# Kernel optimization log

Hardware: AMD Instinct MI355X
Metric: run time of the kernel (lower is better)

The kernel has to match this reference:

```python
import jax, jax.numpy as jnp
import numpy as np

B = 4096          # fused tokens (batch)
E = 1024          # attnConfig embed_size == MoE emb_size
OUT = E // 4      # per-branch feature dim (self.output)
N_EXP = 8         # number of experts
TOP = 2           # top-k routing
H = 8             # attention heads
HD = E // H       # head dim
HID = 4 * E       # expert MLP hidden
IMG = 64 * 64     # flattened single-channel image
W_IMP = 0.01      # importance loss weight


def setup_inputs() -> dict:
    key = jax.random.key(0)
    ks = jax.random.split(key, 24)
    n = lambda i, shp, sc=1.0: jax.random.normal(ks[i], shp, jnp.float32) * sc
    inp = {
        'source': n(0, (B, 1, 64, 64)),
        'target': n(1, (B, 1, 64, 64)),
        'background': n(2, (B, 1, 64, 64)),
        'image': n(3, (B, E)),
        'text': n(4, (B, E)),
        # shared encoder (stub: flatten -> fc to OUT, shared across s/t/b)
        'W_enc': n(5, (IMG, OUT), 0.02), 'b_enc': jnp.zeros((OUT,), jnp.float32),
        # linerImg
        'W_img': n(6, (E, OUT), 0.02), 'b_img': jnp.zeros((OUT,), jnp.float32),
        # cross attention
        'Wq': n(7, (E, E), 0.02), 'bq': jnp.zeros((E,), jnp.float32),
        'Wk': n(8, (E, E), 0.02), 'bk': jnp.zeros((E,), jnp.float32),
        'Wv': n(9, (E, E), 0.02), 'bv': jnp.zeros((E,), jnp.float32),
        'Wo': n(10, (E, E), 0.02), 'bo': jnp.zeros((E,), jnp.float32),
        # gate
        'W_gate': n(11, (E, N_EXP), 0.02), 'b_gate': jnp.zeros((N_EXP,), jnp.float32),
        # experts: per-expert 2-layer MLP E->HID->E
        'W1': n(12, (N_EXP, E, HID), 0.02), 'b1': jnp.zeros((N_EXP, HID), jnp.float32),
        'W2': n(13, (N_EXP, HID, E), 0.02), 'b2': jnp.zeros((N_EXP, E), jnp.float32),
    }
    return inp


def reference(source, target, background, image, text,
              W_enc, b_enc, W_img, b_img,
              Wq, bq, Wk, bk, Wv, bv, Wo, bo,
              W_gate, b_gate, W1, b1, W2, b2):
    enc = lambda a: a.reshape(a.shape[0], -1) @ W_enc + b_enc      # shared_encoder stub
    s = enc(source); t = enc(target); bg = enc(background)        # [B, OUT] each
    img = jax.nn.silu(image @ W_img + b_img)                      # [B, OUT]
    x = jnp.concatenate([s, t, bg, img], axis=1)                  # [B, E] visionFeatures

    # cross attention with seq_len 1 for both x (query) and text (key/value)
    q = (x @ Wq + bq).reshape(B, H, HD)
    k = (text @ Wk + bk).reshape(B, H, HD)
    v = (text @ Wv + bv).reshape(B, H, HD)
    scores = jnp.sum(q * k, axis=-1, keepdims=True) / jnp.sqrt(jnp.float32(HD))  # [B,H,1]
    attw = jax.nn.softmax(scores[..., None], axis=-1)[..., 0]     # softmax over 1 key == 1
    att = (attw * v).reshape(B, E) @ Wo + bo                       # [B, E]

    gate_logits = att @ W_gate + b_gate                            # [B, N_EXP]
    gate_prob = jax.nn.softmax(gate_logits, axis=-1)               # eval mode: no noise
    top_w, top_idx = jax.lax.top_k(gate_prob, TOP)                 # [B, TOP]
    top_w = jax.nn.softmax(top_w, axis=-1)                         # renormalize over top-k

    # dense-dispatch equivalent of the per-expert gather/index_add loop
    h = jax.nn.gelu(jnp.einsum('be,neh->nbh', x, W1) + b1[:, None, :])   # [N,B,HID]
    y_all = jnp.einsum('nbh,nhe->nbe', h, W2) + b2[:, None, :]           # [N,B,E]
    combine = jnp.zeros((B, N_EXP), jnp.float32).at[
        jnp.arange(B)[:, None], top_idx].add(top_w)                      # [B,N]
    y = jnp.einsum('nbe,bn->be', y_all, combine)                          # [B,E]

    importance = gate_prob.sum(axis=0)                             # [N_EXP]
    importance_loss = W_IMP * (jnp.std(importance, ddof=1) / jnp.mean(importance)) ** 2
    return (y, gate_prob, importance_loss)
```

## Files before the change

kernel.cpp:

```cpp
#include <hip/hip_runtime.h>
#include <hip/hip_bf16.h>
#include <stdint.h>

typedef __bf16 bf16_t;
typedef bf16_t bf16x8 __attribute__((ext_vector_type(8)));
typedef float f32x4 __attribute__((ext_vector_type(4)));

static constexpr int B_TOK  = 4096;
static constexpr int E_DIM  = 1024;
static constexpr int N_EXPC = 8;
static constexpr int HID    = 4096;
static constexpr int IMGSZ  = 4096;
static constexpr int NSLOT  = 2 * B_TOK;
static constexpr int NTIL   = 71;

#define DEVI __device__ __forceinline__

DEVI int imin(int a, int b) { return a < b ? a : b; }

DEVI uint16_t f2bf(float f) {
  union { float f; uint32_t u; } v; v.f = f;
  uint32_t u = v.u;
  return (uint16_t)((u + 0x7FFFu + ((u >> 16) & 1u)) >> 16);
}

DEVI void gload_lds16(const void* g, void* l) {
  __builtin_amdgcn_global_load_lds((const __attribute__((address_space(1))) void*)g,
                                   (__attribute__((address_space(3))) void*)l, 16, 0, 0);
}

template<int N> DEVI void waitv() {
  if constexpr (N == 0)       asm volatile("s_waitcnt vmcnt(0)" ::: "memory");
  else if constexpr (N == 2)  asm volatile("s_waitcnt vmcnt(2)" ::: "memory");
  else if constexpr (N == 4)  asm volatile("s_waitcnt vmcnt(4)" ::: "memory");
  else if constexpr (N == 5)  asm volatile("s_waitcnt vmcnt(5)" ::: "memory");
  else if constexpr (N == 8)  asm volatile("s_waitcnt vmcnt(8)" ::: "memory");
  else if constexpr (N == 10) asm volatile("s_waitcnt vmcnt(10)" ::: "memory");
}

#define BAR() do { __builtin_amdgcn_sched_barrier(0); __builtin_amdgcn_s_barrier(); \
                   __builtin_amdgcn_sched_barrier(0); } while (0)

#define MFMA16(a, b, c) __builtin_amdgcn_mfma_f32_16x16x32_bf16((a), (b), (c), 0, 0, 0)

__global__ __launch_bounds__(256)
void transpose64(const float* __restrict__ in, uint16_t* __restrict__ out, int R, int C)
{
  __shared__ float tile[64][65];
  size_t off = (size_t)blockIdx.z * (size_t)R * (size_t)C;
  int c0 = blockIdx.x * 64, r0 = blockIdx.y * 64;
  int t = threadIdx.x;
  #pragma unroll
  for (int i = 0; i < 16; ++i) {
    int rr = i * 4 + (t >> 6), cc = t & 63;
    tile[rr][cc] = in[off + (size_t)(r0 + rr) * C + c0 + cc];
  }
  __syncthreads();
  #pragma unroll
  for (int i = 0; i < 8; ++i) {
    int c = i * 8 + (t >> 5), j = t & 31;
    ushort2 w;
    w.x = f2bf(tile[2 * j][c]);
    w.y = f2bf(tile[2 * j + 1][c]);
    *(ushort2*)&out[off + (size_t)(c0 + c) * R + r0 + 2 * j] = w;
  }
}

template<int BN, int EPI, bool GATHER, bool TILED, int NT>
__global__ __launch_bounds__(256, 3)
void gemm_p(const uint16_t* __restrict__ Ab, int lda,
            const uint16_t* __restrict__ BT, void* __restrict__ Cv, int ldc,
            const float* __restrict__ bias, int K,
            const int* __restrict__ meta, const int* __restrict__ perm,
            size_t bStride, int biasStride)
{
  constexpr int HN = BN / 2, FN = BN / 32;
  constexpr int OPS = (BN == 128 ? 4 : 3);
  int rowBase, rows, e, nt;
  if constexpr (TILED) {
    constexpr int TOTAL = NTIL * NT, Q = TOTAL / 8, FULLB = 64 * NT;
    int bid = blockIdx.x;
    int wg = (bid & 7) * Q + (bid >> 3);
    int mtile;
    if (wg < FULLB) { int rem = wg % (8 * NT); mtile = (wg / (8 * NT)) * 8 + (rem & 7); nt = rem >> 3; }
    else            { int rem = wg - FULLB;    mtile = 64 + rem % 7;                    nt = rem / 7; }
    if (mtile >= meta[0]) return;
    e = meta[1 + 3 * mtile]; rowBase = meta[2 + 3 * mtile]; rows = meta[3 + 3 * mtile];
  } else {
    e = 0; rowBase = blockIdx.x * 128; rows = 128; nt = blockIdx.y;
  }
  const uint16_t* Bt = BT + (TILED ? (size_t)e * bStride : 0);
  const float* bi = bias + (TILED ? (size_t)e * (size_t)biasStride : 0);

  constexpr int ABUF = 8192;
  constexpr int BBUF = (BN == 128) ? 8192 : 4096;
  __shared__ __align__(16) char sAraw[3 * ABUF];
  __shared__ __align__(16) char sBraw[3 * BBUF];

  int t = threadIdx.x, wave = t >> 6, lane = t & 63;
  int wr = wave >> 1, wc = wave & 1;

  int rB = t >> 2;
  int slB = ((t & 3) ^ (rB & 3)) * 8;
  const uint16_t* gB0 = Bt + (size_t)(nt * BN + rB) * K + slB;
  const uint16_t* gB1 = Bt + (size_t)(nt * BN + rB + 64) * K + slB;

  int r0 = t >> 2, r1 = r0 + 64;
  int sl = ((t & 3) ^ (r0 & 3)) * 8;
  int car0, car1;
  if constexpr (TILED) {
    int rr0 = imin(r0, rows - 1), rr1 = imin(r1, rows - 1);
    car0 = GATHER ? perm[rowBase + rr0] : rowBase + rr0;
    car1 = GATHER ? perm[rowBase + rr1] : rowBase + rr1;
  } else { car0 = rowBase + r0; car1 = rowBase + r1; }
  const uint16_t* gA0 = Ab + (size_t)car0 * lda + sl;
  const uint16_t* gA1 = Ab + (size_t)car1 * lda + sl;

  char* laW = sAraw + wave * 1024;
  char* lbW = sBraw + wave * 1024;
  auto STAGE = [&](int kt, int c) {
    int ko = kt << 5;
    char* la = laW + c * ABUF;
    char* lb = lbW + c * BBUF;
    gload_lds16(gA0 + ko, la);
    gload_lds16(gA1 + ko, la + 4096);
    gload_lds16(gB0 + ko, lb);
    if constexpr (BN == 128) gload_lds16(gB1 + ko, lb + 4096);
  };

  f32x4 acc[4][FN];
  #pragma unroll
  for (int m = 0; m < 4; m++)
    #pragma unroll
    for (int n = 0; n < FN; n++)
      acc[m][n] = f32x4{0.f, 0.f, 0.f, 0.f};

  STAGE(0, 0);
  STAGE(1, 1);

  int fr = lane & 15;
  int rdoff = ((lane >> 4) ^ (lane & 3)) * 16;
  int c0 = 0, c2 = 2;
  int nk = K >> 5;

  for (int kt = 0; kt < nk; ++kt) {
    if (kt + 2 < nk) { STAGE(kt + 2, c2); waitv<2 * OPS>(); }
    else if (kt + 1 < nk) waitv<OPS>();
    else waitv<0>();
    BAR();

    const char* bA = sAraw + c0 * ABUF;
    const char* bB = sBraw + c0 * BBUF;
    bf16x8 af[4], bfr[FN];
    #pragma unroll
    for (int m = 0; m < 4; m++)
      af[m] = *(const bf16x8*)(bA + (wr * 64 + m * 16 + fr) * 64 + rdoff);
    #pragma unroll
    for (int n = 0; n < FN; n++)
      bfr[n] = *(const bf16x8*)(bB + (wc * HN + n * 16 + fr) * 64 + rdoff);
    #pragma unroll
    for (int m = 0; m < 4; m++)
      #pragma unroll
      for (int n = 0; n < FN; n++)
        acc[m][n] = MFMA16(af[m], bfr[n], acc[m][n]);

    BAR();
    c0 = (c0 == 2) ? 0 : c0 + 1;
    c2 = (c2 == 2) ? 0 : c2 + 1;
  }

  #pragma unroll
  for (int m = 0; m < 4; m++) {
    int lrow = wr * 64 + m * 16 + (lane >> 4) * 4;
    #pragma unroll
    for (int n = 0; n < FN; n++) {
      int col = nt * BN + wc * HN + n * 16 + (lane & 15);
      float bval = bi[col];
      #pragma unroll
      for (int r = 0; r < 4; r++) {
        int lr = lrow + r;
        if (TILED && lr >= rows) continue;
        float v = acc[m][n][r] + bval;
        size_t cr = (size_t)(rowBase + lr) * ldc + col;
        if (EPI == 3) {
          float u = v + 0.044715f * v * v * v;
          v = v / (1.f + __expf(-1.5957691216057308f * u));
          ((uint16_t*)Cv)[cr] = f2bf(v);
        } else {
          ((float*)Cv)[cr] = v;
        }
      }
    }
  }
}

template<int SPLITK>
__global__ __launch_bounds__(256, 3)
void gemm_encR(const float* __restrict__ F0, const float* __restrict__ F1,
               const float* __restrict__ F2, int lda,
               const uint16_t* __restrict__ BT, float* __restrict__ P, int K)
{
  int z = blockIdx.z, br = z / SPLITK, kc = z % SPLITK;
  const float* Af = (br == 0) ? F0 : (br == 1) ? F1 : F2;
  int Kc = K / SPLITK, k0 = kc * Kc;
  int rowBase = blockIdx.x * 64, nt = blockIdx.y;

  __shared__ __align__(16) char sB[3 * 8192];
  int t = threadIdx.x, wave = t >> 6, lane = t & 63;
  int fr = lane & 15, q4 = lane >> 4;

  const float* gA = Af + (size_t)(rowBase + wave * 16 + fr) * lda + k0 + q4 * 8;

  int rloc = t >> 2;
  int ssw = ((t & 3) ^ (rloc & 3)) * 8;
  const uint16_t* gB0 = BT + (size_t)(nt * 128 + rloc) * K + k0 + ssw;
  const uint16_t* gB1 = gB0 + (size_t)64 * K;

  auto STB = [&](int kt, int c) {
    gload_lds16(gB0 + kt * 32, sB + c * 8192 + wave * 1024);
    gload_lds16(gB1 + kt * 32, sB + c * 8192 + 4096 + wave * 1024);
  };

  f32x4 acc[8];
  #pragma unroll
  for (int n = 0; n < 8; ++n) acc[n] = f32x4{0.f, 0.f, 0.f, 0.f};

  int nk = Kc >> 5;
  STB(0, 0); STB(1, 1);
  f32x4 aE0 = *(const f32x4*)(gA),      aE1 = *(const f32x4*)(gA + 4);
  f32x4 aO0 = *(const f32x4*)(gA + 32), aO1 = *(const f32x4*)(gA + 36);
  int c0 = 0, c2 = 2;
  int bRow = (q4 ^ (fr & 3)) * 16;

  auto step = [&](int kt, f32x4& aX0, f32x4& aX1) {
    bool m2 = kt + 2 < nk;
    if (m2) STB(kt + 2, c2);
    bf16x8 a;
    a[0] = (bf16_t)aX0[0]; a[1] = (bf16_t)aX0[1]; a[2] = (bf16_t)aX0[2]; a[3] = (bf16_t)aX0[3];
    a[4] = (bf16_t)aX1[0]; a[5] = (bf16_t)aX1[1]; a[6] = (bf16_t)aX1[2]; a[7] = (bf16_t)aX1[3];
    int kp = m2 ? kt + 2 : kt;
    aX0 = *(const f32x4*)(gA + kp * 32);
    aX1 = *(const f32x4*)(gA + kp * 32 + 4);
    if (m2) waitv<10>(); else waitv<0>();
    BAR();
    const char* bb = sB + c0 * 8192;
    bf16x8 bfr[8];
    #pragma unroll
    for (int n = 0; n < 8; ++n)
      bfr[n] = *(const bf16x8*)(bb + n * 1024 + fr * 64 + bRow);
    #pragma unroll
    for (int n = 0; n < 8; ++n) acc[n] = MFMA16(a, bfr[n], acc[n]);
    BAR();
    c0 = (c0 == 2) ? 0 : c0 + 1;
    c2 = (c2 == 2) ? 0 : c2 + 1;
  };

  for (int kt = 0; kt < nk; kt += 2) {
    step(kt, aE0, aE1);
    step(kt + 1, aO0, aO1);
  }

  #pragma unroll
  for (int n = 0; n < 8; ++n) {
    int col = nt * 128 + n * 16 + fr;
    #pragma unroll
    for (int r = 0; r < 4; ++r) {
      int row = rowBase + wave * 16 + q4 * 4 + r;
      P[((size_t)z * B_TOK + row) * 256 + col] = acc[n][r];
    }
  }
}

template<int SK, bool SILU>
__global__ __launch_bounds__(256)
void redu_k(const float* __restrict__ P, const float* __restrict__ bias,
            uint16_t* __restrict__ xb, int colBase)
{
  int br = blockIdx.y;
  int row = blockIdx.x * 4 + (threadIdx.x >> 6);
  int c4 = (threadIdx.x & 63) * 4;
  f32x4 s = *(const f32x4*)&bias[c4];
  const float* p = P + ((size_t)br * SK * B_TOK + row) * 256 + c4;
  #pragma unroll
  for (int kc = 0; kc < SK; ++kc)
    s += *(const f32x4*)(p + (size_t)kc * B_TOK * 256);
  if (SILU) {
    #pragma unroll
    for (int j = 0; j < 4; ++j) s[j] = s[j] / (1.f + __expf(-s[j]));
  }
  ushort4 o;
  o.x = f2bf(s[0]); o.y = f2bf(s[1]); o.z = f2bf(s[2]); o.w = f2bf(s[3]);
  *(ushort4*)&xb[(size_t)row * E_DIM + colBase + br * 256 + c4] = o;
}

__global__ __launch_bounds__(256)
void bvwo_k(const float* __restrict__ bv, const float* __restrict__ Wo,
            float* __restrict__ part)
{
  int b = blockIdx.x, t = threadIdx.x;
  f32x4 acc = {0.f, 0.f, 0.f, 0.f};
  for (int k = b * 128; k < b * 128 + 128; ++k) {
    float s = bv[k];
    f32x4 w = *(const f32x4*)&Wo[(size_t)k * E_DIM + t * 4];
    acc[0] = __builtin_fmaf(s, w[0], acc[0]);
    acc[1] = __builtin_fmaf(s, w[1], acc[1]);
    acc[2] = __builtin_fmaf(s, w[2], acc[2]);
    acc[3] = __builtin_fmaf(s, w[3], acc[3]);
  }
  *(f32x4*)&part[(size_t)b * E_DIM + t * 4] = acc;
}

__global__ void t1red_k(const float* __restrict__ part, const float* __restrict__ bo,
                        float* __restrict__ t1)
{
  int j = blockIdx.x * 256 + threadIdx.x;
  float s = bo[j];
  for (int b = 0; b < 8; ++b) s += part[(size_t)b * E_DIM + j];
  t1[j] = s;
}

__global__ __launch_bounds__(256)
void matf_k(const float* __restrict__ W, const float* __restrict__ G,
            float* __restrict__ out)
{
  int k = blockIdx.x * 4 + (threadIdx.x >> 6);
  int lane = threadIdx.x & 63;
  float a0 = 0.f, a1 = 0.f, a2 = 0.f, a3 = 0.f, a4 = 0.f, a5 = 0.f, a6 = 0.f, a7 = 0.f;
  for (int m = lane; m < E_DIM; m += 64) {
    float w = W[(size_t)k * E_DIM + m];
    const float* gm = &G[m * 8];
    a0 = __builtin_fmaf(w, gm[0], a0); a1 = __builtin_fmaf(w, gm[1], a1);
    a2 = __builtin_fmaf(w, gm[2], a2); a3 = __builtin_fmaf(w, gm[3], a3);
    a4 = __builtin_fmaf(w, gm[4], a4); a5 = __builtin_fmaf(w, gm[5], a5);
    a6 = __builtin_fmaf(w, gm[6], a6); a7 = __builtin_fmaf(w, gm[7], a7);
  }
  #pragma unroll
  for (int off = 32; off; off >>= 1) {
    a0 += __shfl_xor(a0, off); a1 += __shfl_xor(a1, off);
    a2 += __shfl_xor(a2, off); a3 += __shfl_xor(a3, off);
    a4 += __shfl_xor(a4, off); a5 += __shfl_xor(a5, off);
    a6 += __shfl_xor(a6, off); a7 += __shfl_xor(a7, off);
  }
  if (lane == 0) {
    float* o = &out[k * 8];
    o[0] = a0; o[1] = a1; o[2] = a2; o[3] = a3;
    o[4] = a4; o[5] = a5; o[6] = a6; o[7] = a7;
  }
}

__global__ __launch_bounds__(512)
void gbias_k(const float* __restrict__ t1, const float* __restrict__ Wg,
             const float* __restrict__ bg, float* __restrict__ gb)
{
  int e = threadIdx.x >> 6, lane = threadIdx.x & 63;
  float s = 0.f;
  for (int m = lane; m < E_DIM; m += 64) s = __builtin_fmaf(t1[m], Wg[m * 8 + e], s);
  #pragma unroll
  for (int off = 32; off; off >>= 1) s += __shfl_xor(s, off);
  if (lane == 0) gb[e] = s + bg[e];
}

__global__ __launch_bounds__(256)
void gate_k(const float* __restrict__ text, const float* __restrict__ G3,
            const float* __restrict__ gb, float* __restrict__ gate_out,
            int* __restrict__ topIdx, float* __restrict__ topW,
            int* __restrict__ counts)
{
  __shared__ __align__(16) float sT[E_DIM];
  __shared__ float lg[8];
  int b = blockIdx.x, t = threadIdx.x;
  *(f32x4*)&sT[t * 4] = *(const f32x4*)&text[(size_t)b * E_DIM + t * 4];
  __syncthreads();
  int wave = t >> 6, lane = t & 63;
  #pragma unroll
  for (int ei = 0; ei < 2; ++ei) {
    int e = wave * 2 + ei;
    float s = 0.f;
    for (int k = lane; k < E_DIM; k += 64) s = __builtin_fmaf(sT[k], G3[k * 8 + e], s);
    #pragma unroll
    for (int off = 32; off; off >>= 1) s += __shfl_down(s, off);
    if (lane == 0) lg[e] = s + gb[e];
  }
  __syncthreads();
  if (t == 0) {
    float p[8];
    float mx = lg[0];
    for (int i = 1; i < 8; i++) mx = fmaxf(mx, lg[i]);
    float den = 0.f;
    for (int i = 0; i < 8; i++) { p[i] = __expf(lg[i] - mx); den += p[i]; }
    float inv = 1.f / den;
    for (int i = 0; i < 8; i++) { p[i] *= inv; gate_out[(size_t)b * 8 + i] = p[i]; }
    int i1 = 0;
    for (int i = 1; i < 8; i++) if (p[i] > p[i1]) i1 = i;
    int i2 = (i1 == 0) ? 1 : 0;
    for (int i = 0; i < 8; i++) if (i != i1 && p[i] > p[i2]) i2 = i;
    float ex = __expf(p[i2] - p[i1]);
    float w1 = 1.f / (1.f + ex), w2 = ex / (1.f + ex);
    topIdx[b * 2] = i1; topIdx[b * 2 + 1] = i2;
    topW[b * 2] = w1;  topW[b * 2 + 1] = w2;
    atomicAdd(&counts[i1], 1);
    atomicAdd(&counts[i2], 1);
  }
}

__global__ void imp_k(const float* __restrict__ gate_out, float* __restrict__ imp)
{
  int e = blockIdx.x, t = threadIdx.x;
  float s = 0.f;
  for (int b = t; b < B_TOK; b += 256) s += gate_out[(size_t)b * 8 + e];
  __shared__ float red[256];
  red[t] = s; __syncthreads();
  for (int off = 128; off; off >>= 1) { if (t < off) red[t] += red[t + off]; __syncthreads(); }
  if (t == 0) imp[e] = red[0];
}

__global__ void loss_k(const float* __restrict__ imp, float* __restrict__ out_loss)
{
  if (threadIdx.x == 0 && blockIdx.x == 0) {
    float m = 0.f;
    for (int e = 0; e < 8; e++) m += imp[e];
    m *= 0.125f;
    float v = 0.f;
    for (int e = 0; e < 8; e++) { float d = imp[e] - m; v += d * d; }
    v /= 7.f;
    out_loss[0] = 0.01f * v / (m * m);
  }
}

__global__ void zero_k(int* counts, int* cursor)
{
  int t = threadIdx.x;
  if (t < 8) { counts[t] = 0; cursor[t] = 0; }
}

__global__ void scan_k(const int* __restrict__ counts, int* __restrict__ bases,
                       int* __restrict__ meta)
{
  if (threadIdx.x == 0) {
    int a = 0, nt = 0;
    for (int e = 0; e < 8; e++) {
      bases[e] = a;
      int c = counts[e];
      for (int j = 0; j < c; j += 128) {
        meta[1 + 3 * nt] = e;
        meta[2 + 3 * nt] = a + j;
        meta[3 + 3 * nt] = (c - j < 128) ? (c - j) : 128;
        nt++;
      }
      a += c;
    }
    meta[0] = nt;
  }
}

__global__ void fill_k(const int* __restrict__ topIdx, int* __restrict__ cursor,
                       const int* __restrict__ bases, int* __restrict__ perm,
                       int* __restrict__ slotOf)
{
  int b = blockIdx.x * 256 + threadIdx.x;
  if (b < B_TOK) {
    #pragma unroll
    for (int j = 0; j < 2; j++) {
      int e = topIdx[b * 2 + j];
      int pos = atomicAdd(&cursor[e], 1);
      int slot = bases[e] + pos;
      perm[slot] = b;
      slotOf[b * 2 + j] = slot;
    }
  }
}

__global__ __launch_bounds__(256)
void combine_k(const float* __restrict__ Yg, const int* __restrict__ slotOf,
               const float* __restrict__ topW, float* __restrict__ y)
{
  int b = blockIdx.x, t = threadIdx.x;
  int s0 = slotOf[b * 2], s1 = slotOf[b * 2 + 1];
  float w0 = topW[b * 2], w1 = topW[b * 2 + 1];
  f32x4 a = *(const f32x4*)&Yg[(size_t)s0 * E_DIM + t * 4];
  f32x4 c = *(const f32x4*)&Yg[(size_t)s1 * E_DIM + t * 4];
  f32x4 r = a * w0 + c * w1;
  *(f32x4*)&y[(size_t)b * E_DIM + t * 4] = r;
}

extern "C" void kernel_launch(void* const* d_in, const int* in_sizes, int n_in,
                              void* d_out, int out_size, void* d_ws, size_t ws_size,
                              hipStream_t stream)
{
  (void)in_sizes; (void)n_in; (void)out_size;
  const float* src   = (const float*)d_in[0];
  const float* tgt   = (const float*)d_in[1];
  const float* bgr   = (const float*)d_in[2];
  const float* image = (const float*)d_in[3];
  const float* text  = (const float*)d_in[4];
  const float* W_enc = (const float*)d_in[5];
  const float* b_enc = (const float*)d_in[6];
  const float* W_img = (const float*)d_in[7];
  const float* b_img = (const float*)d_in[8];
  const float* Wv    = (const float*)d_in[13];
  const float* bv    = (const float*)d_in[14];
  const float* Wo    = (const float*)d_in[15];
  const float* bo    = (const float*)d_in[16];
  const float* Wg    = (const float*)d_in[17];
  const float* bgg   = (const float*)d_in[18];
  const float* W1    = (const float*)d_in[19];
  const float* b1    = (const float*)d_in[20];
  const float* W2    = (const float*)d_in[21];
  const float* b2    = (const float*)d_in[22];

  float* out_y    = (float*)d_out;
  float* out_gate = out_y + (size_t)B_TOK * E_DIM;
  float* out_loss = out_gate + (size_t)B_TOK * N_EXPC;

  char* p = (char*)d_ws;
  auto alloc = [&](size_t bytes) { char* r = p; p += (bytes + 255) & ~(size_t)255; return r; };
  uint16_t* WencT = (uint16_t*)alloc((size_t)256 * IMGSZ * 2);
  uint16_t* WimgT = (uint16_t*)alloc((size_t)256 * E_DIM * 2);
  uint16_t* W1T   = (uint16_t*)alloc((size_t)N_EXPC * HID * E_DIM * 2);
  uint16_t* W2T   = (uint16_t*)alloc((size_t)N_EXPC * E_DIM * HID * 2);
  float* part  = (float*)alloc((size_t)8 * E_DIM * 4);
  float* g1c   = (float*)alloc((size_t)E_DIM * 8 * 4);
  float* G3    = (float*)alloc((size_t)E_DIM * 8 * 4);
  float* t1    = (float*)alloc(E_DIM * 4);
  float* gbv   = (float*)alloc(64 * 4);
  float* impb  = (float*)alloc(64 * 4);
  int*   topIdx = (int*)alloc(B_TOK * 2 * 4);
  float* topW   = (float*)alloc(B_TOK * 2 * 4);
  int*   slotOf = (int*)alloc(B_TOK * 2 * 4);
  int*   counts = (int*)alloc(64 * 4);
  int*   bases  = (int*)alloc(64 * 4);
  int*   cursor = (int*)alloc(64 * 4);
  int*   meta   = (int*)alloc((1 + 3 * (NTIL + 1)) * 4 + 64);
  int*   perm   = (int*)alloc(NSLOT * 4);
  uint16_t* xbf  = (uint16_t*)alloc((size_t)B_TOK * E_DIM * 2);
  uint16_t* Hbuf = (uint16_t*)alloc((size_t)NSLOT * HID * 2);
  char* uni = alloc((size_t)14 * B_TOK * 256 * 4);
  float* Penc = (float*)uni;
  float* Pimg = Penc + (size_t)12 * B_TOK * 256;
  float* Yg   = (float*)uni;
  if ((size_t)(p - (char*)d_ws) > ws_size) return;

  zero_k<<<1, 64, 0, stream>>>(counts, cursor);

  transpose64<<<dim3(256 / 64, IMGSZ / 64, 1), 256, 0, stream>>>(W_enc, WencT, IMGSZ, 256);
  transpose64<<<dim3(256 / 64, E_DIM / 64, 1), 256, 0, stream>>>(W_img, WimgT, E_DIM, 256);
  transpose64<<<dim3(HID / 64, E_DIM / 64, 8), 256, 0, stream>>>(W1, W1T, E_DIM, HID);
  transpose64<<<dim3(E_DIM / 64, HID / 64, 8), 256, 0, stream>>>(W2, W2T, HID, E_DIM);

  bvwo_k<<<8, 256, 0, stream>>>(bv, Wo, part);
  t1red_k<<<4, 256, 0, stream>>>(part, bo, t1);
  matf_k<<<256, 256, 0, stream>>>(Wo, Wg, g1c);
  matf_k<<<256, 256, 0, stream>>>(Wv, g1c, G3);
  gbias_k<<<1, 512, 0, stream>>>(t1, Wg, bgg, gbv);
  gate_k<<<B_TOK, 256, 0, stream>>>(text, G3, gbv, out_gate, topIdx, topW, counts);
  imp_k<<<8, 256, 0, stream>>>(out_gate, impb);
  loss_k<<<1, 64, 0, stream>>>(impb, out_loss);
  scan_k<<<1, 64, 0, stream>>>(counts, bases, meta);
  fill_k<<<16, 256, 0, stream>>>(topIdx, cursor, bases, perm, slotOf);

  gemm_encR<4><<<dim3(B_TOK / 64, 2, 12), 256, 0, stream>>>(
      src, tgt, bgr, IMGSZ, WencT, Penc, IMGSZ);
  gemm_encR<2><<<dim3(B_TOK / 64, 2, 2), 256, 0, stream>>>(
      image, image, image, E_DIM, WimgT, Pimg, E_DIM);
  redu_k<4, false><<<dim3(B_TOK / 4, 3), 256, 0, stream>>>(Penc, b_enc, xbf, 0);
  redu_k<2, true><<<dim3(B_TOK / 4, 1), 256, 0, stream>>>(Pimg, b_img, xbf, 768);

  gemm_p<128, 3, true, true, HID / 128><<<dim3(NTIL * (HID / 128)), 256, 0, stream>>>(
      xbf, E_DIM, W1T, Hbuf, HID, b1, E_DIM, meta, perm, (size_t)HID * E_DIM, HID);
  gemm_p<128, 0, false, true, E_DIM / 128><<<dim3(NTIL * (E_DIM / 128)), 256, 0, stream>>>(
      Hbuf, HID, W2T, Yg, E_DIM, b2, HID, meta, perm, (size_t)E_DIM * HID, E_DIM);

  combine_k<<<B_TOK, 256, 0, stream>>>(Yg, slotOf, topW, out_y);
}
```

Baseline: 697.7 us.

## Split-K the expert down-projection, double-buffer GEMM, and vectorize transpose loads

The second expert GEMM (H @ W2) gets a 2-way K split so the grid has twice as many workgroups. Each half writes its own fp32 partial plane, and combine_k sums the planes and adds b2 per expert. The GEMM pipeline drops from triple to double buffering with a smaller LDS footprint, and launch bounds rise to 5 waves per SIMD for higher occupancy. The weight transpose now reads float4 instead of scalars. In exchange there is extra partial-sum memory traffic and less prefetch depth to hide latency.

```diff
diff --git a/kernel.cpp b/kernel.cpp
--- a/kernel.cpp
+++ b/kernel.cpp
@@ -31,10 +31,8 @@
 
 template<int N> DEVI void waitv() {
   if constexpr (N == 0)       asm volatile("s_waitcnt vmcnt(0)" ::: "memory");
-  else if constexpr (N == 2)  asm volatile("s_waitcnt vmcnt(2)" ::: "memory");
+  else if constexpr (N == 3)  asm volatile("s_waitcnt vmcnt(3)" ::: "memory");
   else if constexpr (N == 4)  asm volatile("s_waitcnt vmcnt(4)" ::: "memory");
-  else if constexpr (N == 5)  asm volatile("s_waitcnt vmcnt(5)" ::: "memory");
-  else if constexpr (N == 8)  asm volatile("s_waitcnt vmcnt(8)" ::: "memory");
   else if constexpr (N == 10) asm volatile("s_waitcnt vmcnt(10)" ::: "memory");
 }
 
@@ -51,9 +49,11 @@
   int c0 = blockIdx.x * 64, r0 = blockIdx.y * 64;
   int t = threadIdx.x;
   #pragma unroll
-  for (int i = 0; i < 16; ++i) {
-    int rr = i * 4 + (t >> 6), cc = t & 63;
-    tile[rr][cc] = in[off + (size_t)(r0 + rr) * C + c0 + cc];
+  for (int i = 0; i < 4; ++i) {
+    int rr = i * 16 + (t >> 4), c4 = (t & 15) * 4;
+    f32x4 v = *(const f32x4*)&in[off + (size_t)(r0 + rr) * C + c0 + c4];
+    tile[rr][c4 + 0] = v[0]; tile[rr][c4 + 1] = v[1];
+    tile[rr][c4 + 2] = v[2]; tile[rr][c4 + 3] = v[3];
   }
   __syncthreads();
   #pragma unroll
@@ -66,55 +66,50 @@
   }
 }
 
-template<int BN, int EPI, bool GATHER, bool TILED, int NT>
-__global__ __launch_bounds__(256, 3)
+template<int BN, int EPI, bool GATHER, int NT, int KSPLIT>
+__global__ __launch_bounds__(256, 5)
 void gemm_p(const uint16_t* __restrict__ Ab, int lda,
             const uint16_t* __restrict__ BT, void* __restrict__ Cv, int ldc,
             const float* __restrict__ bias, int K,
             const int* __restrict__ meta, const int* __restrict__ perm,
-            size_t bStride, int biasStride)
+            size_t bStride, int biasStride, size_t cPlane)
 {
   constexpr int HN = BN / 2, FN = BN / 32;
   constexpr int OPS = (BN == 128 ? 4 : 3);
-  int rowBase, rows, e, nt;
-  if constexpr (TILED) {
-    constexpr int TOTAL = NTIL * NT, Q = TOTAL / 8, FULLB = 64 * NT;
-    int bid = blockIdx.x;
-    int wg = (bid & 7) * Q + (bid >> 3);
-    int mtile;
-    if (wg < FULLB) { int rem = wg % (8 * NT); mtile = (wg / (8 * NT)) * 8 + (rem & 7); nt = rem >> 3; }
-    else            { int rem = wg - FULLB;    mtile = 64 + rem % 7;                    nt = rem / 7; }
-    if (mtile >= meta[0]) return;
-    e = meta[1 + 3 * mtile]; rowBase = meta[2 + 3 * mtile]; rows = meta[3 + 3 * mtile];
-  } else {
-    e = 0; rowBase = blockIdx.x * 128; rows = 128; nt = blockIdx.y;
-  }
-  const uint16_t* Bt = BT + (TILED ? (size_t)e * bStride : 0);
-  const float* bi = bias + (TILED ? (size_t)e * (size_t)biasStride : 0);
+  constexpr int NT2 = NT * KSPLIT;
+  constexpr int TOTAL = NTIL * NT2, Q = TOTAL / 8, FULLB = 64 * NT2;
+  int bid = blockIdx.x;
+  int wg = (bid & 7) * Q + (bid >> 3);
+  int mtile, nt2;
+  if (wg < FULLB) { int rem = wg % (8 * NT2); mtile = (wg / (8 * NT2)) * 8 + (rem & 7); nt2 = rem >> 3; }
+  else            { int rem = wg - FULLB;     mtile = 64 + rem % 7;                     nt2 = rem / 7; }
+  if (mtile >= meta[0]) return;
+  int nt = nt2 % NT, kc = nt2 / NT;
+  int e = meta[1 + 3 * mtile], rowBase = meta[2 + 3 * mtile], rows = meta[3 + 3 * mtile];
+  int Kc = K / KSPLIT, k0 = kc * Kc;
+  const uint16_t* Bt = BT + (size_t)e * bStride;
+  const float* bi = bias + (size_t)e * (size_t)biasStride;
 
   constexpr int ABUF = 8192;
   constexpr int BBUF = (BN == 128) ? 8192 : 4096;
-  __shared__ __align__(16) char sAraw[3 * ABUF];
-  __shared__ __align__(16) char sBraw[3 * BBUF];
+  __shared__ __align__(16) char sAraw[2 * ABUF];
+  __shared__ __align__(16) char sBraw[2 * BBUF];
 
   int t = threadIdx.x, wave = t >> 6, lane = t & 63;
   int wr = wave >> 1, wc = wave & 1;
 
   int rB = t >> 2;
   int slB = ((t & 3) ^ (rB & 3)) * 8;
-  const uint16_t* gB0 = Bt + (size_t)(nt * BN + rB) * K + slB;
-  const uint16_t* gB1 = Bt + (size_t)(nt * BN + rB + 64) * K + slB;
+  const uint16_t* gB0 = Bt + (size_t)(nt * BN + rB) * K + k0 + slB;
+  const uint16_t* gB1 = Bt + (size_t)(nt * BN + rB + 64) * K + k0 + slB;
 
   int r0 = t >> 2, r1 = r0 + 64;
   int sl = ((t & 3) ^ (r0 & 3)) * 8;
-  int car0, car1;
-  if constexpr (TILED) {
-    int rr0 = imin(r0, rows - 1), rr1 = imin(r1, rows - 1);
-    car0 = GATHER ? perm[rowBase + rr0] : rowBase + rr0;
-    car1 = GATHER ? perm[rowBase + rr1] : rowBase + rr1;
-  } else { car0 = rowBase + r0; car1 = rowBase + r1; }
-  const uint16_t* gA0 = Ab + (size_t)car0 * lda + sl;
-  const uint16_t* gA1 = Ab + (size_t)car1 * lda + sl;
+  int rr0 = imin(r0, rows - 1), rr1 = imin(r1, rows - 1);
+  int car0 = GATHER ? perm[rowBase + rr0] : rowBase + rr0;
+  int car1 = GATHER ? perm[rowBase + rr1] : rowBase + rr1;
+  const uint16_t* gA0 = Ab + (size_t)car0 * lda + k0 + sl;
+  const uint16_t* gA1 = Ab + (size_t)car1 * lda + k0 + sl;
 
   char* laW = sAraw + wave * 1024;
   char* lbW = sBraw + wave * 1024;
@@ -136,21 +131,20 @@
       acc[m][n] = f32x4{0.f, 0.f, 0.f, 0.f};
 
   STAGE(0, 0);
-  STAGE(1, 1);
 
   int fr = lane & 15;
   int rdoff = ((lane >> 4) ^ (lane & 3)) * 16;
-  int c0 = 0, c2 = 2;
-  int nk = K >> 5;
+  int nk = Kc >> 5;
 
   for (int kt = 0; kt < nk; ++kt) {
-    if (kt + 2 < nk) { STAGE(kt + 2, c2); waitv<2 * OPS>(); }
-    else if (kt + 1 < nk) waitv<OPS>();
+    int b = kt & 1, nb = b ^ 1;
+    bool more = kt + 1 < nk;
+    if (more) { STAGE(kt + 1, nb); waitv<OPS>(); }
     else waitv<0>();
     BAR();
 
-    const char* bA = sAraw + c0 * ABUF;
-    const char* bB = sBraw + c0 * BBUF;
+    const char* bA = sAraw + b * ABUF;
+    const char* bB = sBraw + b * BBUF;
     bf16x8 af[4], bfr[FN];
     #pragma unroll
     for (int m = 0; m < 4; m++)
@@ -165,8 +159,6 @@
         acc[m][n] = MFMA16(af[m], bfr[n], acc[m][n]);
 
     BAR();
-    c0 = (c0 == 2) ? 0 : c0 + 1;
-    c2 = (c2 == 2) ? 0 : c2 + 1;
   }
 
   #pragma unroll
@@ -175,13 +167,13 @@
     #pragma unroll
     for (int n = 0; n < FN; n++) {
       int col = nt * BN + wc * HN + n * 16 + (lane & 15);
-      float bval = bi[col];
+      float bval = (EPI == 3) ? bi[col] : 0.f;
       #pragma unroll
       for (int r = 0; r < 4; r++) {
         int lr = lrow + r;
-        if (TILED && lr >= rows) continue;
+        if (lr >= rows) continue;
         float v = acc[m][n][r] + bval;
-        size_t cr = (size_t)(rowBase + lr) * ldc + col;
+        size_t cr = (size_t)kc * cPlane + (size_t)(rowBase + lr) * ldc + col;
         if (EPI == 3) {
           float u = v + 0.044715f * v * v * v;
           v = v / (1.f + __expf(-1.5957691216057308f * u));
@@ -471,16 +463,24 @@
 }
 
 __global__ __launch_bounds__(256)
-void combine_k(const float* __restrict__ Yg, const int* __restrict__ slotOf,
-               const float* __restrict__ topW, float* __restrict__ y)
+void combine_k(const float* __restrict__ Yp, const int* __restrict__ slotOf,
+               const int* __restrict__ topIdx, const float* __restrict__ topW,
+               const float* __restrict__ b2, float* __restrict__ y)
 {
   int b = blockIdx.x, t = threadIdx.x;
   int s0 = slotOf[b * 2], s1 = slotOf[b * 2 + 1];
+  int e0 = topIdx[b * 2], e1 = topIdx[b * 2 + 1];
   float w0 = topW[b * 2], w1 = topW[b * 2 + 1];
-  f32x4 a = *(const f32x4*)&Yg[(size_t)s0 * E_DIM + t * 4];
-  f32x4 c = *(const f32x4*)&Yg[(size_t)s1 * E_DIM + t * 4];
-  f32x4 r = a * w0 + c * w1;
-  *(f32x4*)&y[(size_t)b * E_DIM + t * 4] = r;
+  int c = t * 4;
+  size_t P1 = (size_t)NSLOT * E_DIM;
+  f32x4 x0 = *(const f32x4*)&Yp[(size_t)s0 * E_DIM + c];
+  x0 += *(const f32x4*)&Yp[P1 + (size_t)s0 * E_DIM + c];
+  x0 += *(const f32x4*)&b2[(size_t)e0 * E_DIM + c];
+  f32x4 x1 = *(const f32x4*)&Yp[(size_t)s1 * E_DIM + c];
+  x1 += *(const f32x4*)&Yp[P1 + (size_t)s1 * E_DIM + c];
+  x1 += *(const f32x4*)&b2[(size_t)e1 * E_DIM + c];
+  f32x4 r = x0 * w0 + x1 * w1;
+  *(f32x4*)&y[(size_t)b * E_DIM + c] = r;
 }
 
 extern "C" void kernel_launch(void* const* d_in, const int* in_sizes, int n_in,
@@ -534,10 +534,10 @@
   int*   perm   = (int*)alloc(NSLOT * 4);
   uint16_t* xbf  = (uint16_t*)alloc((size_t)B_TOK * E_DIM * 2);
   uint16_t* Hbuf = (uint16_t*)alloc((size_t)NSLOT * HID * 2);
-  char* uni = alloc((size_t)14 * B_TOK * 256 * 4);
+  char* uni = alloc((size_t)2 * NSLOT * E_DIM * 4);
   float* Penc = (float*)uni;
   float* Pimg = Penc + (size_t)12 * B_TOK * 256;
-  float* Yg   = (float*)uni;
+  float* Yp   = (float*)uni;
   if ((size_t)(p - (char*)d_ws) > ws_size) return;
 
   zero_k<<<1, 64, 0, stream>>>(counts, cursor);
@@ -565,10 +565,11 @@
   redu_k<4, false><<<dim3(B_TOK / 4, 3), 256, 0, stream>>>(Penc, b_enc, xbf, 0);
   redu_k<2, true><<<dim3(B_TOK / 4, 1), 256, 0, stream>>>(Pimg, b_img, xbf, 768);
 
-  gemm_p<128, 3, true, true, HID / 128><<<dim3(NTIL * (HID / 128)), 256, 0, stream>>>(
-      xbf, E_DIM, W1T, Hbuf, HID, b1, E_DIM, meta, perm, (size_t)HID * E_DIM, HID);
-  gemm_p<128, 0, false, true, E_DIM / 128><<<dim3(NTIL * (E_DIM / 128)), 256, 0, stream>>>(
-      Hbuf, HID, W2T, Yg, E_DIM, b2, HID, meta, perm, (size_t)E_DIM * HID, E_DIM);
-
-  combine_k<<<B_TOK, 256, 0, stream>>>(Yg, slotOf, topW, out_y);
-}
+  gemm_p<128, 3, true, HID / 128, 1><<<dim3(NTIL * (HID / 128)), 256, 0, stream>>>(
+      xbf, E_DIM, W1T, Hbuf, HID, b1, E_DIM, meta, perm, (size_t)HID * E_DIM, HID, 0);
+  gemm_p<128, 0, false, E_DIM / 128, 2><<<dim3(NTIL * (E_DIM / 128) * 2), 256, 0, stream>>>(
+      Hbuf, HID, W2T, Yp, E_DIM, b2, HID, meta, perm, (size_t)E_DIM * HID, E_DIM,
+      (size_t)NSLOT * E_DIM);
+
+  combine_k<<<B_TOK, 256, 0, stream>>>(Yp, slotOf, topIdx, topW, b2, out_y);
+}
```

Measured after the change: 715.8 us. 1.03x slower.
